# Kernel tuning notes

Hardware: AMD Instinct MI355X
Metric: run time of the kernel (lower is better)

The kernel has to match this reference:

```python
import jax, jax.numpy as jnp
import numpy as np

N_QUBITS = 6
N_LAYERS = 3
DIM = 2 ** N_QUBITS  # 64

# PauliZ sign table: signs[s, q] = +1 if bit q of basis state s is 0 else -1
# (wire 0 is the most-significant bit, matching pennylane default.qubit)
_IDX = np.arange(DIM)
SIGNS = np.stack([1.0 - 2.0 * ((_IDX >> (N_QUBITS - 1 - q)) & 1) for q in range(N_QUBITS)], axis=1).astype(np.float32)  # (64, 6)


def _rx_mat(theta):  # theta: (B,) -> (B,2,2) complex64
    c = jnp.cos(theta / 2).astype(jnp.complex64)
    s = (-1j * jnp.sin(theta / 2)).astype(jnp.complex64)
    return jnp.stack([jnp.stack([c, s], -1), jnp.stack([s, c], -1)], -2)


def _ry_mat(theta):  # theta: (B,) -> (B,2,2) complex64
    c = jnp.cos(theta / 2).astype(jnp.complex64)
    s = jnp.sin(theta / 2).astype(jnp.complex64)
    return jnp.stack([jnp.stack([c, -s], -1), jnp.stack([s, c], -1)], -2)


def _rz_mat(theta):  # theta: (B,) -> (B,2,2) complex64 (diagonal)
    z = jnp.zeros_like(theta).astype(jnp.complex64)
    e0 = jnp.exp(-1j * theta.astype(jnp.complex64) / 2)
    e1 = jnp.exp(1j * theta.astype(jnp.complex64) / 2)
    return jnp.stack([jnp.stack([e0, z], -1), jnp.stack([z, e1], -1)], -2)


def _apply_1q(state, U, w):
    # state: (B, 64); U: (B,2,2) batched or (2,2) shared; gate on wire w
    B = state.shape[0]
    st = state.reshape(B, 2 ** w, 2, 2 ** (N_QUBITS - 1 - w))
    if U.ndim == 3:
        st = jnp.einsum('bij,bajc->baic', U, st)
    else:
        st = jnp.einsum('ij,bajc->baic', U, st)
    return st.reshape(B, DIM)


def _cnot(state, c, t):
    # CNOT with control wire c, target wire t (fixed structure, batched over B)
    B = state.shape[0]
    s = state.reshape((B,) + (2,) * N_QUBITS)
    ac, at = c + 1, t + 1
    s0 = jnp.take(s, 0, axis=ac)
    s1 = jnp.take(s, 1, axis=ac)
    at2 = at - 1 if at > ac else at  # axis shift after removing control axis
    s1 = jnp.flip(s1, axis=at2)      # X on target when control == 1
    s = jnp.stack([s0, s1], axis=ac)
    return s.reshape(B, DIM)


def simulate(x6, q_weights):
    # x6: (B, 6) angles; q_weights: (3, 6). Returns PauliZ expvals (B, 6).
    B = x6.shape[0]
    state = jnp.zeros((B, DIM), dtype=jnp.complex64).at[:, 0].set(1.0)
    # input encoding: RX, RY, RZ on each wire with rolled input angles
    for i in range(N_QUBITS):
        state = _apply_1q(state, _rx_mat(x6[:, i % N_QUBITS]), i)
        state = _apply_1q(state, _ry_mat(x6[:, (i + 1) % N_QUBITS]), i)
        state = _apply_1q(state, _rz_mat(x6[:, (i + 2) % N_QUBITS]), i)
    # variational layers: RY(weights) then ring of CNOTs
    for l in range(N_LAYERS):
        for q in range(N_QUBITS):
            th = q_weights[l, q]
            c = jnp.cos(th / 2).astype(jnp.complex64)
            s = jnp.sin(th / 2).astype(jnp.complex64)
            U = jnp.stack([jnp.stack([c, -s]), jnp.stack([s, c])])  # (2,2)
            state = _apply_1q(state, U, q)
        for q in range(N_QUBITS):
            state = _cnot(state, q, (q + 1) % N_QUBITS)
    probs = (state.real ** 2 + state.imag ** 2)  # (B, 64) float32
    return probs @ jnp.asarray(SIGNS)            # (B, 6)


def setup_inputs() -> dict:
    key = jax.random.key(0)
    k1, k2, k3, k4 = jax.random.split(key, 4)
    B, H = 32768, 1024
    x = jax.random.normal(k1, (B, N_QUBITS), dtype=jnp.float32)
    hx = jax.random.normal(k2, (B, H), dtype=jnp.float32)
    q_weights = jax.random.uniform(k3, (N_LAYERS, N_QUBITS), dtype=jnp.float32, minval=0.0, maxval=2.0 * np.pi)
    bound = 1.0 / np.sqrt(N_QUBITS)
    fc_w = jax.random.uniform(k4, (H, N_QUBITS), dtype=jnp.float32, minval=-bound, maxval=bound)
    fc_b = jax.random.uniform(jax.random.fold_in(k4, 1), (H,), dtype=jnp.float32, minval=-bound, maxval=bound)
    return {"x": x, "hx": hx, "q_weights": q_weights, "fc_w": fc_w, "fc_b": fc_b}


def reference(x, hx, q_weights, fc_w, fc_b):
    q = simulate(x[:, :N_QUBITS], q_weights)      # (B, 6) PauliZ expvals
    return hx + q @ fc_w.T + fc_b                 # residual + linear
```

## Files before the change

### kernel.cpp

```cpp
#include <hip/hip_runtime.h>


#define NQ 6

typedef float floatx4 __attribute__((ext_vector_type(4)));

__global__ __launch_bounds__(256, 4) void qrnn_fused_kernel(
    const float* __restrict__ x,
    const float* __restrict__ hx,
    const float* __restrict__ qw,
    const float* __restrict__ fc_w,
    const float* __restrict__ fc_b,
    float* __restrict__ out)
{
    const int tid = threadIdx.x;
    const int l   = tid & 63;
    const int wv  = tid >> 6;
    const int bid = blockIdx.x;
    const int G   = gridDim.x;

    __shared__ float q6s[4][6];

    const float4* hx4 = (const float4*)hx;
    float4 hv0 = hx4[(size_t)(bid + 0 * G) * 256 + tid];
    float4 hv1 = hx4[(size_t)(bid + 1 * G) * 256 + tid];
    float4 hv2 = hx4[(size_t)(bid + 2 * G) * 256 + tid];
    float4 hv3 = hx4[(size_t)(bid + 3 * G) * 256 + tid];
    const float4* w4 = (const float4*)fc_w;
    const int wb = tid * 6;
    float4 a0 = w4[wb + 0], a1 = w4[wb + 1], a2 = w4[wb + 2];
    float4 a3 = w4[wb + 3], a4 = w4[wb + 4], a5 = w4[wb + 5];
    float4 bv = ((const float4*)fc_b)[tid];

    const int b = bid + wv * G;

    float ang = 0.f;
    if (l < 6)        ang = x[(size_t)b * NQ + l];
    else if (l < 24)  ang = qw[l - 6];
    float sa, ca;
    __sincosf(ang * 0.5f, &sa, &ca);

    float cx[6], sx[6];
    #pragma unroll
    for (int i = 0; i < 6; ++i) { cx[i] = __shfl(ca, i); sx[i] = __shfl(sa, i); }

    float re = (l == 0) ? 1.f : 0.f;
    float im = 0.f;

    #pragma unroll
    for (int w = 0; w < 6; ++w) {
        const int m = 1 << (5 - w);
        const float sgn = (l & m) ? 1.f : -1.f;
        float pr = __shfl_xor(re, m), pi = __shfl_xor(im, m);
        float c = cx[w], s = sx[w];
        float nr = c * re + s * pi;
        float ni = c * im - s * pr;
        re = nr; im = ni;
        pr = __shfl_xor(re, m); pi = __shfl_xor(im, m);
        c = cx[(w + 1) % 6]; s = sx[(w + 1) % 6] * sgn;
        nr = c * re + s * pr;
        ni = c * im + s * pi;
        re = nr; im = ni;
        c = cx[(w + 2) % 6];
        const float sg = (l & m) ? -sx[(w + 2) % 6] : sx[(w + 2) % 6];
        nr = c * re + sg * im;
        ni = c * im - sg * re;
        re = nr; im = ni;
    }

    int src = l;
    #pragma unroll
    for (int q = 5; q >= 0; --q) {
        const int cb = 5 - q, tb = 5 - ((q + 1) % 6);
        src ^= ((src >> cb) & 1) << tb;
    }

    #pragma unroll
    for (int lay = 0; lay < 3; ++lay) {
        #pragma unroll
        for (int q = 0; q < 6; ++q) {
            const int m = 1 << (5 - q);
            const float c = __shfl(ca, 6 + lay * 6 + q);
            const float s = __shfl(sa, 6 + lay * 6 + q);
            const float sg = (l & m) ? s : -s;
            const float pr = __shfl_xor(re, m), pi = __shfl_xor(im, m);
            const float nr = c * re + sg * pr;
            const float ni = c * im + sg * pi;
            re = nr; im = ni;
        }
        re = __shfl(re, src);
        im = __shfl(im, src);
    }

    float p = re * re + im * im;
    #pragma unroll
    for (int k = 0; k < 6; ++k) {
        const int m = 1 << k;
        const float t = __shfl_xor(p, m);
        p = (l & m) ? (t - p) : (t + p);
    }
    const int srcl = (l < 6) ? (32 >> l) : 0;
    const float v = __shfl(p, srcl);
    if (l < 6) q6s[wv][l] = v;
    __syncthreads();

    floatx4* out4 = (floatx4*)out;
    #pragma unroll
    for (int k = 0; k < 4; ++k) {
        const float* qb = q6s[k];
        const float q0 = qb[0], q1 = qb[1], q2 = qb[2];
        const float q3 = qb[3], q4 = qb[4], q5 = qb[5];
        const float4 hvk = (k == 0) ? hv0 : (k == 1) ? hv1 : (k == 2) ? hv2 : hv3;
        floatx4 res;
        res.x = hvk.x + bv.x + q0*a0.x + q1*a0.y + q2*a0.z + q3*a0.w + q4*a1.x + q5*a1.y;
        res.y = hvk.y + bv.y + q0*a1.z + q1*a1.w + q2*a2.x + q3*a2.y + q4*a2.z + q5*a2.w;
        res.z = hvk.z + bv.z + q0*a3.x + q1*a3.y + q2*a3.z + q3*a3.w + q4*a4.x + q5*a4.y;
        res.w = hvk.w + bv.w + q0*a4.z + q1*a4.w + q2*a5.x + q3*a5.y + q4*a5.z + q5*a5.w;
        __builtin_nontemporal_store(res, &out4[(size_t)(bid + k * G) * 256 + tid]);
    }
}

extern "C" void kernel_launch(void* const* d_in, const int* in_sizes, int n_in,
                              void* d_out, int out_size, void* d_ws, size_t ws_size,
                              hipStream_t stream) {
    const float* x    = (const float*)d_in[0];
    const float* hx   = (const float*)d_in[1];
    const float* qw   = (const float*)d_in[2];
    const float* fc_w = (const float*)d_in[3];
    const float* fc_b = (const float*)d_in[4];
    float* out = (float*)d_out;

    const int B = in_sizes[0] / NQ;

    qrnn_fused_kernel<<<B / 4, 256, 0, stream>>>(x, hx, qw, fc_w, fc_b, out);
}
```

Measured before the change: 244.8 us.

## Process 16 rows per block in a loop, reusing fc weights and layer trig

Each block now handles 16 batch rows over 4 loop iterations instead of 4 rows, with a quarter as many blocks. The fc_w/fc_b loads and the variational-layer sincos values are computed once per block and kept in registers, using readlane to broadcast them as scalars instead of shuffles. Rows are now contiguous per block rather than strided by grid size, and a double-buffered shared array limits the barriers to one per iteration. The trade-off is fewer blocks (less parallelism for latency hiding) and serialised iterations in which hx loads are only partly overlapped with the simulation.

```diff
diff --git a/kernel.cpp b/kernel.cpp
--- a/kernel.cpp
+++ b/kernel.cpp
@@ -4,6 +4,10 @@
 #define NQ 6
 
 typedef float floatx4 __attribute__((ext_vector_type(4)));
+
+__device__ __forceinline__ float rl(float v, int lane) {
+    return __int_as_float(__builtin_amdgcn_readlane(__float_as_int(v), lane));
+}
 
 __global__ __launch_bounds__(256, 4) void qrnn_fused_kernel(
     const float* __restrict__ x,
@@ -17,56 +21,27 @@
     const int l   = tid & 63;
     const int wv  = tid >> 6;
     const int bid = blockIdx.x;
-    const int G   = gridDim.x;
 
-    __shared__ float q6s[4][6];
+    __shared__ float q6s[2][4][6];
 
-    const float4* hx4 = (const float4*)hx;
-    float4 hv0 = hx4[(size_t)(bid + 0 * G) * 256 + tid];
-    float4 hv1 = hx4[(size_t)(bid + 1 * G) * 256 + tid];
-    float4 hv2 = hx4[(size_t)(bid + 2 * G) * 256 + tid];
-    float4 hv3 = hx4[(size_t)(bid + 3 * G) * 256 + tid];
     const float4* w4 = (const float4*)fc_w;
-    const int wb = tid * 6;
-    float4 a0 = w4[wb + 0], a1 = w4[wb + 1], a2 = w4[wb + 2];
-    float4 a3 = w4[wb + 3], a4 = w4[wb + 4], a5 = w4[wb + 5];
-    float4 bv = ((const float4*)fc_b)[tid];
+    const int h4 = wv * 64 + l;
+    const int wb = h4 * 6;
+    const float4 a0 = w4[wb + 0], a1 = w4[wb + 1], a2 = w4[wb + 2];
+    const float4 a3 = w4[wb + 3], a4 = w4[wb + 4], a5 = w4[wb + 5];
+    const float4 bv = ((const float4*)fc_b)[h4];
 
-    const int b = bid + wv * G;
-
-    float ang = 0.f;
-    if (l < 6)        ang = x[(size_t)b * NQ + l];
-    else if (l < 24)  ang = qw[l - 6];
-    float sa, ca;
-    __sincosf(ang * 0.5f, &sa, &ca);
-
-    float cx[6], sx[6];
+    float angq = (l >= 6 && l < 24) ? qw[l - 6] : 0.f;
+    float saq, caq;
+    __sincosf(angq * 0.5f, &saq, &caq);
+    float cQ[3][6], sQ[3][6];
     #pragma unroll
-    for (int i = 0; i < 6; ++i) { cx[i] = __shfl(ca, i); sx[i] = __shfl(sa, i); }
-
-    float re = (l == 0) ? 1.f : 0.f;
-    float im = 0.f;
-
-    #pragma unroll
-    for (int w = 0; w < 6; ++w) {
-        const int m = 1 << (5 - w);
-        const float sgn = (l & m) ? 1.f : -1.f;
-        float pr = __shfl_xor(re, m), pi = __shfl_xor(im, m);
-        float c = cx[w], s = sx[w];
-        float nr = c * re + s * pi;
-        float ni = c * im - s * pr;
-        re = nr; im = ni;
-        pr = __shfl_xor(re, m); pi = __shfl_xor(im, m);
-        c = cx[(w + 1) % 6]; s = sx[(w + 1) % 6] * sgn;
-        nr = c * re + s * pr;
-        ni = c * im + s * pi;
-        re = nr; im = ni;
-        c = cx[(w + 2) % 6];
-        const float sg = (l & m) ? -sx[(w + 2) % 6] : sx[(w + 2) % 6];
-        nr = c * re + sg * im;
-        ni = c * im - sg * re;
-        re = nr; im = ni;
-    }
+    for (int lay = 0; lay < 3; ++lay)
+        #pragma unroll
+        for (int q = 0; q < 6; ++q) {
+            cQ[lay][q] = rl(caq, 6 + lay * 6 + q);
+            sQ[lay][q] = rl(saq, 6 + lay * 6 + q);
+        }
 
     int src = l;
     #pragma unroll
@@ -74,49 +49,94 @@
         const int cb = 5 - q, tb = 5 - ((q + 1) % 6);
         src ^= ((src >> cb) & 1) << tb;
     }
+    const int srcl = (l < 6) ? (32 >> l) : 0;
 
-    #pragma unroll
-    for (int lay = 0; lay < 3; ++lay) {
+    const float4* hx4 = (const float4*)hx;
+    floatx4* out4 = (floatx4*)out;
+
+    #pragma unroll 1
+    for (int it = 0; it < 4; ++it) {
+        const int r0 = bid * 16 + it * 4;
+        const int b  = r0 + wv;
+
+        const float angx = (l < 6) ? x[(size_t)b * NQ + l] : 0.f;
+
+        float4 hv0 = hx4[(size_t)(r0 + 0) * 256 + h4];
+        float4 hv1 = hx4[(size_t)(r0 + 1) * 256 + h4];
+        float4 hv2 = hx4[(size_t)(r0 + 2) * 256 + h4];
+        float4 hv3 = hx4[(size_t)(r0 + 3) * 256 + h4];
+
+        float sax, cax;
+        __sincosf(angx * 0.5f, &sax, &cax);
+        float cx[6], sx[6];
         #pragma unroll
-        for (int q = 0; q < 6; ++q) {
-            const int m = 1 << (5 - q);
-            const float c = __shfl(ca, 6 + lay * 6 + q);
-            const float s = __shfl(sa, 6 + lay * 6 + q);
-            const float sg = (l & m) ? s : -s;
-            const float pr = __shfl_xor(re, m), pi = __shfl_xor(im, m);
-            const float nr = c * re + sg * pr;
-            const float ni = c * im + sg * pi;
+        for (int i = 0; i < 6; ++i) { cx[i] = rl(cax, i); sx[i] = rl(sax, i); }
+
+        float re = (l == 0) ? 1.f : 0.f;
+        float im = 0.f;
+
+        #pragma unroll
+        for (int w = 0; w < 6; ++w) {
+            const int m = 1 << (5 - w);
+            const float sgn = (l & m) ? 1.f : -1.f;
+            float pr = __shfl_xor(re, m), pi = __shfl_xor(im, m);
+            float c = cx[w], s = sx[w];
+            float nr = c * re + s * pi;
+            float ni = c * im - s * pr;
+            re = nr; im = ni;
+            pr = __shfl_xor(re, m); pi = __shfl_xor(im, m);
+            c = cx[(w + 1) % 6]; s = sx[(w + 1) % 6] * sgn;
+            nr = c * re + s * pr;
+            ni = c * im + s * pi;
+            re = nr; im = ni;
+            c = cx[(w + 2) % 6];
+            const float sg = (l & m) ? -sx[(w + 2) % 6] : sx[(w + 2) % 6];
+            nr = c * re + sg * im;
+            ni = c * im - sg * re;
             re = nr; im = ni;
         }
-        re = __shfl(re, src);
-        im = __shfl(im, src);
-    }
 
-    float p = re * re + im * im;
-    #pragma unroll
-    for (int k = 0; k < 6; ++k) {
-        const int m = 1 << k;
-        const float t = __shfl_xor(p, m);
-        p = (l & m) ? (t - p) : (t + p);
-    }
-    const int srcl = (l < 6) ? (32 >> l) : 0;
-    const float v = __shfl(p, srcl);
-    if (l < 6) q6s[wv][l] = v;
-    __syncthreads();
+        #pragma unroll
+        for (int lay = 0; lay < 3; ++lay) {
+            #pragma unroll
+            for (int q = 0; q < 6; ++q) {
+                const int m = 1 << (5 - q);
+                const float c = cQ[lay][q];
+                const float s = sQ[lay][q];
+                const float sg = (l & m) ? s : -s;
+                const float pr = __shfl_xor(re, m), pi = __shfl_xor(im, m);
+                const float nr = c * re + sg * pr;
+                const float ni = c * im + sg * pi;
+                re = nr; im = ni;
+            }
+            re = __shfl(re, src);
+            im = __shfl(im, src);
+        }
 
-    floatx4* out4 = (floatx4*)out;
-    #pragma unroll
-    for (int k = 0; k < 4; ++k) {
-        const float* qb = q6s[k];
-        const float q0 = qb[0], q1 = qb[1], q2 = qb[2];
-        const float q3 = qb[3], q4 = qb[4], q5 = qb[5];
-        const float4 hvk = (k == 0) ? hv0 : (k == 1) ? hv1 : (k == 2) ? hv2 : hv3;
-        floatx4 res;
-        res.x = hvk.x + bv.x + q0*a0.x + q1*a0.y + q2*a0.z + q3*a0.w + q4*a1.x + q5*a1.y;
-        res.y = hvk.y + bv.y + q0*a1.z + q1*a1.w + q2*a2.x + q3*a2.y + q4*a2.z + q5*a2.w;
-        res.z = hvk.z + bv.z + q0*a3.x + q1*a3.y + q2*a3.z + q3*a3.w + q4*a4.x + q5*a4.y;
-        res.w = hvk.w + bv.w + q0*a4.z + q1*a4.w + q2*a5.x + q3*a5.y + q4*a5.z + q5*a5.w;
-        __builtin_nontemporal_store(res, &out4[(size_t)(bid + k * G) * 256 + tid]);
+        float p = re * re + im * im;
+        #pragma unroll
+        for (int k = 0; k < 6; ++k) {
+            const int m = 1 << k;
+            const float t = __shfl_xor(p, m);
+            p = (l & m) ? (t - p) : (t + p);
+        }
+        const float v = __shfl(p, srcl);
+        if (l < 6) q6s[it & 1][wv][l] = v;
+        __syncthreads();
+
+        #pragma unroll
+        for (int r = 0; r < 4; ++r) {
+            const float* qb = q6s[it & 1][r];
+            const float q0 = qb[0], q1 = qb[1], q2 = qb[2];
+            const float q3 = qb[3], q4 = qb[4], q5 = qb[5];
+            const float4 hvk = (r == 0) ? hv0 : (r == 1) ? hv1 : (r == 2) ? hv2 : hv3;
+            floatx4 res;
+            res.x = hvk.x + bv.x + q0*a0.x + q1*a0.y + q2*a0.z + q3*a0.w + q4*a1.x + q5*a1.y;
+            res.y = hvk.y + bv.y + q0*a1.z + q1*a1.w + q2*a2.x + q3*a2.y + q4*a2.z + q5*a2.w;
+            res.z = hvk.z + bv.z + q0*a3.x + q1*a3.y + q2*a3.z + q3*a3.w + q4*a4.x + q5*a4.y;
+            res.w = hvk.w + bv.w + q0*a4.z + q1*a4.w + q2*a5.x + q3*a5.y + q4*a5.z + q5*a5.w;
+            __builtin_nontemporal_store(res, &out4[(size_t)(r0 + r) * 256 + h4]);
+        }
     }
 }
 
@@ -132,5 +152,5 @@
 
     const int B = in_sizes[0] / NQ;
 
-    qrnn_fused_kernel<<<B / 4, 256, 0, stream>>>(x, hx, qw, fc_w, fc_b, out);
+    qrnn_fused_kernel<<<B / 16, 256, 0, stream>>>(x, hx, qw, fc_w, fc_b, out);
 }
```

Measured after the change: 248.6 us. Within noise of the previous version (+1.5%).

## Split fused kernel into simulation kernel and persistent streaming epilogue kernel

Applied to the files above, without the earlier changes.

Splits the work into two kernels. The first runs the 6-qubit simulation per batch row and writes the six expectation values to workspace. The second is a grid-stride epilogue with 2048 blocks that loads fc_w and fc_b once per thread and streams hx to out row by row. Angle broadcasts now use readlane instead of shuffles. The aim is to separate the compute-heavy simulation from the bandwidth-bound stream and to reuse the weight registers across rows. The cost is an extra launch, a workspace round trip, and the loss of the earlier overlap between the hx loads and the simulation.

```diff
diff --git a/kernel.cpp b/kernel.cpp
--- a/kernel.cpp
+++ b/kernel.cpp
@@ -5,34 +5,19 @@
 
 typedef float floatx4 __attribute__((ext_vector_type(4)));
 
-__global__ __launch_bounds__(256, 4) void qrnn_fused_kernel(
+__device__ __forceinline__ float rl(float v, int lane) {
+    return __int_as_float(__builtin_amdgcn_readlane(__float_as_int(v), lane));
+}
+
+__global__ __launch_bounds__(256, 4) void qrnn_sim_kernel(
     const float* __restrict__ x,
-    const float* __restrict__ hx,
     const float* __restrict__ qw,
-    const float* __restrict__ fc_w,
-    const float* __restrict__ fc_b,
-    float* __restrict__ out)
+    float* __restrict__ q6)
 {
     const int tid = threadIdx.x;
     const int l   = tid & 63;
     const int wv  = tid >> 6;
-    const int bid = blockIdx.x;
-    const int G   = gridDim.x;
-
-    __shared__ float q6s[4][6];
-
-    const float4* hx4 = (const float4*)hx;
-    float4 hv0 = hx4[(size_t)(bid + 0 * G) * 256 + tid];
-    float4 hv1 = hx4[(size_t)(bid + 1 * G) * 256 + tid];
-    float4 hv2 = hx4[(size_t)(bid + 2 * G) * 256 + tid];
-    float4 hv3 = hx4[(size_t)(bid + 3 * G) * 256 + tid];
-    const float4* w4 = (const float4*)fc_w;
-    const int wb = tid * 6;
-    float4 a0 = w4[wb + 0], a1 = w4[wb + 1], a2 = w4[wb + 2];
-    float4 a3 = w4[wb + 3], a4 = w4[wb + 4], a5 = w4[wb + 5];
-    float4 bv = ((const float4*)fc_b)[tid];
-
-    const int b = bid + wv * G;
+    const int b   = blockIdx.x * 4 + wv;
 
     float ang = 0.f;
     if (l < 6)        ang = x[(size_t)b * NQ + l];
@@ -42,7 +27,7 @@
 
     float cx[6], sx[6];
     #pragma unroll
-    for (int i = 0; i < 6; ++i) { cx[i] = __shfl(ca, i); sx[i] = __shfl(sa, i); }
+    for (int i = 0; i < 6; ++i) { cx[i] = rl(ca, i); sx[i] = rl(sa, i); }
 
     float re = (l == 0) ? 1.f : 0.f;
     float im = 0.f;
@@ -80,8 +65,8 @@
         #pragma unroll
         for (int q = 0; q < 6; ++q) {
             const int m = 1 << (5 - q);
-            const float c = __shfl(ca, 6 + lay * 6 + q);
-            const float s = __shfl(sa, 6 + lay * 6 + q);
+            const float c = rl(ca, 6 + lay * 6 + q);
+            const float s = rl(sa, 6 + lay * 6 + q);
             const float sg = (l & m) ? s : -s;
             const float pr = __shfl_xor(re, m), pi = __shfl_xor(im, m);
             const float nr = c * re + sg * pr;
@@ -101,22 +86,41 @@
     }
     const int srcl = (l < 6) ? (32 >> l) : 0;
     const float v = __shfl(p, srcl);
-    if (l < 6) q6s[wv][l] = v;
-    __syncthreads();
+    if (l < 6) q6[(size_t)b * NQ + l] = v;
+}
 
+__global__ __launch_bounds__(256) void qrnn_epi_kernel(
+    const float* __restrict__ hx,
+    const float* __restrict__ q6,
+    const float* __restrict__ fc_w,
+    const float* __restrict__ fc_b,
+    float* __restrict__ out,
+    int B)
+{
+    const int tid = threadIdx.x;
+    const int nb  = gridDim.x;
+
+    const float4* w4 = (const float4*)fc_w;
+    const int wb = tid * 6;
+    const float4 a0 = w4[wb + 0], a1 = w4[wb + 1], a2 = w4[wb + 2];
+    const float4 a3 = w4[wb + 3], a4 = w4[wb + 4], a5 = w4[wb + 5];
+    const float4 bv = ((const float4*)fc_b)[tid];
+
+    const float4* hx4 = (const float4*)hx;
     floatx4* out4 = (floatx4*)out;
-    #pragma unroll
-    for (int k = 0; k < 4; ++k) {
-        const float* qb = q6s[k];
-        const float q0 = qb[0], q1 = qb[1], q2 = qb[2];
-        const float q3 = qb[3], q4 = qb[4], q5 = qb[5];
-        const float4 hvk = (k == 0) ? hv0 : (k == 1) ? hv1 : (k == 2) ? hv2 : hv3;
+
+    for (int row = blockIdx.x; row < B; row += nb) {
+        const float* qr = q6 + (size_t)row * NQ;
+        const float q0 = qr[0], q1 = qr[1], q2 = qr[2];
+        const float q3 = qr[3], q4 = qr[4], q5 = qr[5];
+
+        const float4 hv = hx4[(size_t)row * 256 + tid];
         floatx4 res;
-        res.x = hvk.x + bv.x + q0*a0.x + q1*a0.y + q2*a0.z + q3*a0.w + q4*a1.x + q5*a1.y;
-        res.y = hvk.y + bv.y + q0*a1.z + q1*a1.w + q2*a2.x + q3*a2.y + q4*a2.z + q5*a2.w;
-        res.z = hvk.z + bv.z + q0*a3.x + q1*a3.y + q2*a3.z + q3*a3.w + q4*a4.x + q5*a4.y;
-        res.w = hvk.w + bv.w + q0*a4.z + q1*a4.w + q2*a5.x + q3*a5.y + q4*a5.z + q5*a5.w;
-        __builtin_nontemporal_store(res, &out4[(size_t)(bid + k * G) * 256 + tid]);
+        res.x = hv.x + bv.x + q0*a0.x + q1*a0.y + q2*a0.z + q3*a0.w + q4*a1.x + q5*a1.y;
+        res.y = hv.y + bv.y + q0*a1.z + q1*a1.w + q2*a2.x + q3*a2.y + q4*a2.z + q5*a2.w;
+        res.z = hv.z + bv.z + q0*a3.x + q1*a3.y + q2*a3.z + q3*a3.w + q4*a4.x + q5*a4.y;
+        res.w = hv.w + bv.w + q0*a4.z + q1*a4.w + q2*a5.x + q3*a5.y + q4*a5.z + q5*a5.w;
+        __builtin_nontemporal_store(res, &out4[(size_t)row * 256 + tid]);
     }
 }
 
@@ -132,5 +136,8 @@
 
     const int B = in_sizes[0] / NQ;
 
-    qrnn_fused_kernel<<<B / 4, 256, 0, stream>>>(x, hx, qw, fc_w, fc_b, out);
+    float* q6 = (float*)d_ws;
+
+    qrnn_sim_kernel<<<B / 4, 256, 0, stream>>>(x, qw, q6);
+    qrnn_epi_kernel<<<2048, 256, 0, stream>>>(hx, q6, fc_w, fc_b, out, B);
 }
```

Result: slower. 273.9 us (+11.9%).
